# Optimization experiments

Hardware: AMD Instinct MI355X
Metric: run time of the kernel (lower is better)

The kernel has to match this reference:

```python
import jax, jax.numpy as jnp
import numpy as np

N, D, K = 131072, 64, 512
COMMITMENT_COST = 0.25
DECAY = 0.99
EPSILON = 1e-05


def setup_inputs() -> dict:
    key = jax.random.key(0)
    k1, k2, k3 = jax.random.split(key, 3)
    return {
        "inputs": jax.random.normal(k1, (N, D), dtype=jnp.float32),
        "embedding_weight": jax.random.normal(k2, (K, D), dtype=jnp.float32),
        "ema_w": jax.random.normal(k3, (K, D), dtype=jnp.float32),
        "ema_cluster_size": jnp.zeros((K,), dtype=jnp.float32),
    }


def reference(inputs, embedding_weight, ema_w, ema_cluster_size):
    num_embeddings = embedding_weight.shape[0]
    distances = (
        jnp.sum(inputs ** 2, axis=1, keepdims=True)
        + jnp.sum(embedding_weight ** 2, axis=1)
        - 2.0 * jnp.matmul(inputs, embedding_weight.T)
    )
    encoding_indices = jnp.argmin(distances, axis=1)  # [N]
    # dense one-hot (returned by the module); float32 instead of torch double
    encodings = jax.nn.one_hot(encoding_indices, num_embeddings, dtype=jnp.float32)
    # encodings @ W is just a codebook gather
    quantized = jnp.take(embedding_weight, encoding_indices, axis=0)  # [N, D]

    # ---- EMA codebook update (training path; all detached from autodiff) ----
    counts = jax.ops.segment_sum(
        jnp.ones((inputs.shape[0],), dtype=jnp.float32),
        encoding_indices, num_segments=num_embeddings)  # == encodings.sum(0)
    new_cluster_size = ema_cluster_size * DECAY + (1.0 - DECAY) * counts
    n = jnp.sum(new_cluster_size)
    new_cluster_size = (new_cluster_size + EPSILON) / (n + num_embeddings * EPSILON) * n
    # dw = encodings^T @ inputs -> scatter-add of inputs per code
    dw = jax.ops.segment_sum(inputs, encoding_indices, num_segments=num_embeddings)
    new_ema_w = ema_w * DECAY + (1.0 - DECAY) * dw
    new_embedding = new_ema_w / new_cluster_size[:, None]
    new_cluster_size = jax.lax.stop_gradient(new_cluster_size)
    new_ema_w = jax.lax.stop_gradient(new_ema_w)
    new_embedding = jax.lax.stop_gradient(new_embedding)

    # commitment loss (quantized detached)
    e_latent_loss = jnp.mean((jax.lax.stop_gradient(quantized) - inputs) ** 2)
    loss = COMMITMENT_COST * e_latent_loss
    # straight-through estimator
    quantized_st = inputs + jax.lax.stop_gradient(quantized - inputs)

    avg_probs = jnp.mean(encodings, axis=0)
    perplexity = jnp.exp(-jnp.sum(avg_probs * jnp.log(avg_probs + 1e-10)))
    return (loss, quantized_st, perplexity, encodings,
            new_embedding, new_cluster_size, new_ema_w)
```

## Files before the change

kernel.cpp:

```cpp
#include <hip/hip_runtime.h>

#define NROWS 131072
#define DDIM  64
#define KCODE 512

#define QUANT_OFF 1LL
#define PERP_OFF  8388609LL
#define ENC_OFF   8388610LL
#define EMB_OFF   75497474LL
#define CS_OFF    75530242LL
#define EMAW_OFF  75530754LL

#define WS_COUNTS 0
#define WS_NEGWN  512
#define WS_SSE    1024
#define WS_DW     1040
#define WS_ZERO_FLOATS 33808
#define WS_OFF    33808
#define WS_POS    34320
#define WS_IDX    34832
#define WS_BUCKET 165904
#define WS_WHI    296976
#define WS_WMID   313360
#define WS_WLO    329744

using short8 = __attribute__((ext_vector_type(8))) short;
using f32x4  = __attribute__((ext_vector_type(4))) float;

#define MFMA(a, b, c) __builtin_amdgcn_mfma_f32_16x16x32_bf16((a), (b), (c), 0, 0, 0)

__device__ inline unsigned short bf16_rne(float x) {
    unsigned u = __float_as_uint(x);
    unsigned r = u + 0x7FFFu + ((u >> 16) & 1u);
    return (unsigned short)(r >> 16);
}
__device__ inline float bf16_to_f(unsigned short h) {
    return __uint_as_float((unsigned)h << 16);
}
__device__ inline void split3(const float* v, short8& h8, short8& m8, short8& l8) {
#pragma unroll
    for (int j = 0; j < 8; ++j) {
        float x = v[j];
        unsigned short h = bf16_rne(x);
        float m_ = x - bf16_to_f(h);
        unsigned short m = bf16_rne(m_);
        float l_ = m_ - bf16_to_f(m);
        unsigned short l = bf16_rne(l_);
        h8[j] = (short)h; m8[j] = (short)m; l8[j] = (short)l;
    }
}

__global__ void wnorm_kernel(const float* __restrict__ W, float* __restrict__ negwn) {
    int k = threadIdx.x;
    const float4* wr = reinterpret_cast<const float4*>(&W[(size_t)k * DDIM]);
    float s = 0.f;
#pragma unroll
    for (int i = 0; i < DDIM / 4; ++i) {
        float4 v = wr[i];
        s += v.x * v.x + v.y * v.y + v.z * v.z + v.w * v.w;
    }
    negwn[k] = -0.5f * s;
}

__global__ void wprep_kernel(const float* __restrict__ W, ushort* __restrict__ whi,
                             ushort* __restrict__ wmid, ushort* __restrict__ wlo) {
    int t = blockIdx.x * 256 + threadIdx.x;
    int lane = t & 63;
    int code = (t >> 6) * 16 + (lane & 15);
    int kbase = (lane >> 4) * 8;
    int obase = t * 16;
#pragma unroll
    for (int kh = 0; kh < 2; ++kh) {
        float xbuf[8];
#pragma unroll
        for (int j = 0; j < 8; ++j) xbuf[j] = W[code * 64 + kh * 32 + kbase + j];
        short8 h8, m8, l8;
        split3(xbuf, h8, m8, l8);
#pragma unroll
        for (int j = 0; j < 8; ++j) {
            whi[obase + kh * 8 + j]  = (ushort)h8[j];
            wmid[obase + kh * 8 + j] = (ushort)m8[j];
            wlo[obase + kh * 8 + j]  = (ushort)l8[j];
        }
    }
}

__global__ __launch_bounds__(256) void vq_main_kernel(
    const float* __restrict__ X, const ushort* __restrict__ WHI,
    const ushort* __restrict__ WMID, const ushort* __restrict__ WLO,
    const float* __restrict__ negwn, const float* __restrict__ W,
    float* __restrict__ counts, float* __restrict__ sse_g,
    int* __restrict__ idx_out, float* __restrict__ outq, float* __restrict__ enc) {

    __shared__ int rowIdx[128];
    const int tid = threadIdx.x;
    const int wave = tid >> 6, lane = tid & 63;
    const int col = lane & 15, kg = lane >> 4;
    const int row0 = blockIdx.x * 128;
    const int rowbase = row0 + wave * 32;

    short8 xh[2][2], xm[2][2], xl[2][2];
#pragma unroll
    for (int t = 0; t < 2; ++t) {
        int row = rowbase + t * 16 + col;
#pragma unroll
        for (int kh = 0; kh < 2; ++kh) {
            const float4* p = reinterpret_cast<const float4*>(&X[row * 64 + kh * 32 + kg * 8]);
            float4 a = p[0], b = p[1];
            float xbuf[8] = {a.x, a.y, a.z, a.w, b.x, b.y, b.z, b.w};
            split3(xbuf, xh[t][kh], xm[t][kh], xl[t][kh]);
        }
    }

    float bestV[2][4]; int bestC[2][4];
#pragma unroll
    for (int t = 0; t < 2; ++t)
#pragma unroll
        for (int i = 0; i < 4; ++i) { bestV[t][i] = -3.4e38f; bestC[t][i] = 0; }

    for (int c = 0; c < 32; ++c) {
        const short8* ph = reinterpret_cast<const short8*>(&WHI[(c * 64 + lane) * 16]);
        const short8* pm = reinterpret_cast<const short8*>(&WMID[(c * 64 + lane) * 16]);
        const short8* pl = reinterpret_cast<const short8*>(&WLO[(c * 64 + lane) * 16]);
        short8 wh0 = ph[0], wh1 = ph[1];
        short8 wm0 = pm[0], wm1 = pm[1];
        short8 wl0 = pl[0], wl1 = pl[1];
        float wn = negwn[c * 16 + col];
#pragma unroll
        for (int t = 0; t < 2; ++t) {
            f32x4 acc = {0.f, 0.f, 0.f, 0.f};
            acc = MFMA(xh[t][0], wl0, acc); acc = MFMA(xh[t][1], wl1, acc);
            acc = MFMA(xl[t][0], wh0, acc); acc = MFMA(xl[t][1], wh1, acc);
            acc = MFMA(xm[t][0], wm0, acc); acc = MFMA(xm[t][1], wm1, acc);
            acc = MFMA(xh[t][0], wm0, acc); acc = MFMA(xh[t][1], wm1, acc);
            acc = MFMA(xm[t][0], wh0, acc); acc = MFMA(xm[t][1], wh1, acc);
            acc = MFMA(xh[t][0], wh0, acc); acc = MFMA(xh[t][1], wh1, acc);
#pragma unroll
            for (int i = 0; i < 4; ++i) {
                float r = acc[i] + wn;
                if (r > bestV[t][i]) { bestV[t][i] = r; bestC[t][i] = c; }
            }
        }
    }

#pragma unroll
    for (int t = 0; t < 2; ++t)
#pragma unroll
        for (int i = 0; i < 4; ++i) {
            float v = bestV[t][i];
            int ix = bestC[t][i] * 16 + col;
#pragma unroll
            for (int m = 1; m <= 8; m <<= 1) {
                float ov = __shfl_xor(v, m);
                int   oi = __shfl_xor(ix, m);
                if (ov > v || (ov == v && oi < ix)) { v = ov; ix = oi; }
            }
            if (col == 0) rowIdx[wave * 32 + t * 16 + kg * 4 + i] = ix;
        }
    __syncthreads();

    float ssel = 0.f;
    for (int u = tid; u < 128 * 16; u += 256) {
        int r = u >> 4, d4 = (u & 15) << 2;
        int ix = rowIdx[r];
        float4 wv = *reinterpret_cast<const float4*>(&W[ix * 64 + d4]);
        float4 xv = *reinterpret_cast<const float4*>(&X[(size_t)(row0 + r) * 64 + d4]);
        float dx = wv.x - xv.x, dy = wv.y - xv.y, dz = wv.z - xv.z, dw4 = wv.w - xv.w;
        ssel += dx * dx + dy * dy + dz * dz + dw4 * dw4;
        size_t ob = (size_t)(row0 + r) * 64 + d4;
        outq[ob + 0] = xv.x + dx;
        outq[ob + 1] = xv.y + dy;
        outq[ob + 2] = xv.z + dz;
        outq[ob + 3] = xv.w + dw4;
    }
#pragma unroll
    for (int m = 32; m >= 1; m >>= 1) ssel += __shfl_xor(ssel, m);
    if (lane == 0) atomicAdd(sse_g, ssel);

    if (tid < 128) {
        int ix = rowIdx[tid];
        idx_out[row0 + tid] = ix;
        atomicAdd(&counts[ix], 1.0f);
        enc[(size_t)(row0 + tid) * KCODE + ix] = 1.0f;
    }
}

__global__ void prefix_kernel(const float* __restrict__ counts,
                              int* __restrict__ off, int* __restrict__ pos) {
    __shared__ int tmp[512];
    int t = threadIdx.x;
    int c = (int)counts[t];
    tmp[t] = c;
    __syncthreads();
    int val = c;
    for (int s = 1; s < 512; s <<= 1) {
        int add = (t >= s) ? tmp[t - s] : 0;
        __syncthreads();
        val += add; tmp[t] = val;
        __syncthreads();
    }
    int excl = val - c;
    off[t] = excl; pos[t] = excl;
}

__global__ void scatter_kernel(const int* __restrict__ idx, int* __restrict__ pos,
                               int* __restrict__ bucket) {
    int i = blockIdx.x * 256 + threadIdx.x;
    int k = idx[i];
    int p = atomicAdd(&pos[k], 1);
    bucket[p] = (k << 17) | i;
}

__global__ __launch_bounds__(256) void dwsum_kernel(
    const float* __restrict__ X, const int* __restrict__ bucket,
    float* __restrict__ dw) {
    const int lane = threadIdx.x & 63;
    const int gwave = (blockIdx.x * 256 + threadIdx.x) >> 6;
    const int r0 = gwave * 16;
    int v = bucket[r0];
    int k = v >> 17, row = v & 0x1FFFF;
    float acc = 0.f;
#pragma unroll
    for (int i = 0; i < 16; ++i) {
        acc += X[(size_t)row * 64 + lane];
        if (i + 1 < 16) {
            int nv = bucket[r0 + i + 1];
            int nk = nv >> 17, nrow = nv & 0x1FFFF;
            if (nk != k) {
                atomicAdd(&dw[k * 64 + lane], acc);
                acc = 0.f; k = nk;
            }
            row = nrow;
        }
    }
    atomicAdd(&dw[k * 64 + lane], acc);
}

__global__ __launch_bounds__(512) void finalize_kernel(
    const float* __restrict__ ema_w, const float* __restrict__ ema_cs,
    const float* __restrict__ counts, const float* __restrict__ dw,
    const float* __restrict__ sse_g, float* __restrict__ out) {

    __shared__ float red[512];
    __shared__ float cs_sh[512];
    int t = threadIdx.x;

    float cnt = counts[t];
    float raw = ema_cs[t] * 0.99f + 0.01f * cnt;
    red[t] = raw;
    __syncthreads();
    for (int s = 256; s > 0; s >>= 1) {
        if (t < s) red[t] += red[t + s];
        __syncthreads();
    }
    float n = red[0];
    __syncthreads();

    float ncs = (raw + 1e-5f) / (n + (float)KCODE * 1e-5f) * n;
    out[CS_OFF + t] = ncs;
    cs_sh[t] = ncs;

    float avg = cnt / (float)NROWS;
    red[t] = avg * logf(avg + 1e-10f);
    __syncthreads();
    for (int s = 256; s > 0; s >>= 1) {
        if (t < s) red[t] += red[t + s];
        __syncthreads();
    }
    if (t == 0) {
        out[PERP_OFF] = expf(-red[0]);
        out[0] = 0.25f * sse_g[0] / ((float)NROWS * (float)DDIM);
    }
    __syncthreads();

    for (int i = t; i < KCODE * DDIM; i += 512) {
        float ne = ema_w[i] * 0.99f + 0.01f * dw[i];
        out[EMAW_OFF + i] = ne;
        out[EMB_OFF + i] = ne / cs_sh[i >> 6];
    }
}

extern "C" void kernel_launch(void* const* d_in, const int* in_sizes, int n_in,
                              void* d_out, int out_size, void* d_ws, size_t ws_size,
                              hipStream_t stream) {
    const float* X      = (const float*)d_in[0];
    const float* W      = (const float*)d_in[1];
    const float* ema_w  = (const float*)d_in[2];
    const float* ema_cs = (const float*)d_in[3];
    float* out = (float*)d_out;
    float* ws  = (float*)d_ws;

    float*  counts = ws + WS_COUNTS;
    float*  negwn  = ws + WS_NEGWN;
    float*  sse    = ws + WS_SSE;
    float*  dw     = ws + WS_DW;
    int*    off    = (int*)(ws + WS_OFF);
    int*    pos    = (int*)(ws + WS_POS);
    int*    idx    = (int*)(ws + WS_IDX);
    int*    bucket = (int*)(ws + WS_BUCKET);
    ushort* whi    = (ushort*)(ws + WS_WHI);
    ushort* wmid   = (ushort*)(ws + WS_WMID);
    ushort* wlo    = (ushort*)(ws + WS_WLO);

    hipMemsetAsync(d_ws, 0, (size_t)WS_ZERO_FLOATS * sizeof(float), stream);
    hipMemsetAsync(out + ENC_OFF, 0, (size_t)NROWS * KCODE * sizeof(float), stream);

    wnorm_kernel<<<1, 512, 0, stream>>>(W, negwn);
    wprep_kernel<<<8, 256, 0, stream>>>(W, whi, wmid, wlo);
    vq_main_kernel<<<NROWS / 128, 256, 0, stream>>>(X, whi, wmid, wlo, negwn, W,
                                                    counts, sse, idx,
                                                    out + QUANT_OFF, out + ENC_OFF);
    prefix_kernel<<<1, 512, 0, stream>>>(counts, off, pos);
    scatter_kernel<<<NROWS / 256, 256, 0, stream>>>(idx, pos, bucket);
    dwsum_kernel<<<NROWS / 16 / 4, 256, 0, stream>>>(X, bucket, dw);
    finalize_kernel<<<1, 512, 0, stream>>>(ema_w, ema_cs, counts, dw, sse, out);
}
```

Measured before the change: 298.8 us.

## Write one-hot encodings densely in main kernel and merge weight prep kernels

Drops the 256 MiB memset of the encodings buffer and has each block of the main kernel write its own 128x512 one-hot tile in full, using 16-byte nontemporal stores. The base offset is only 8-byte aligned, so the head and tail pairs are handled separately. This removes one full write pass over the largest output. The codebook norm and bf16 split kernels are also merged into a single launch. The cost is extra store work and LDS index comparisons inside the main kernel.

```diff
diff --git a/kernel.cpp b/kernel.cpp
--- a/kernel.cpp
+++ b/kernel.cpp
@@ -26,6 +26,7 @@
 
 using short8 = __attribute__((ext_vector_type(8))) short;
 using f32x4  = __attribute__((ext_vector_type(4))) float;
+using f32x2  = __attribute__((ext_vector_type(2))) float;
 
 #define MFMA(a, b, c) __builtin_amdgcn_mfma_f32_16x16x32_bf16((a), (b), (c), 0, 0, 0)
 
@@ -50,20 +51,23 @@
     }
 }
 
-__global__ void wnorm_kernel(const float* __restrict__ W, float* __restrict__ negwn) {
-    int k = threadIdx.x;
-    const float4* wr = reinterpret_cast<const float4*>(&W[(size_t)k * DDIM]);
-    float s = 0.f;
-#pragma unroll
-    for (int i = 0; i < DDIM / 4; ++i) {
-        float4 v = wr[i];
-        s += v.x * v.x + v.y * v.y + v.z * v.z + v.w * v.w;
-    }
-    negwn[k] = -0.5f * s;
-}
-
-__global__ void wprep_kernel(const float* __restrict__ W, ushort* __restrict__ whi,
-                             ushort* __restrict__ wmid, ushort* __restrict__ wlo) {
+__global__ __launch_bounds__(256) void prep_kernel(
+    const float* __restrict__ W, ushort* __restrict__ whi,
+    ushort* __restrict__ wmid, ushort* __restrict__ wlo,
+    float* __restrict__ negwn) {
+    if (blockIdx.x == 8) {
+        for (int k = threadIdx.x; k < KCODE; k += 256) {
+            const float4* wr = reinterpret_cast<const float4*>(&W[(size_t)k * DDIM]);
+            float s = 0.f;
+#pragma unroll
+            for (int i = 0; i < DDIM / 4; ++i) {
+                float4 v = wr[i];
+                s += v.x * v.x + v.y * v.y + v.z * v.z + v.w * v.w;
+            }
+            negwn[k] = -0.5f * s;
+        }
+        return;
+    }
     int t = blockIdx.x * 256 + threadIdx.x;
     int lane = t & 63;
     int code = (t >> 6) * 16 + (lane & 15);
@@ -181,7 +185,35 @@
         int ix = rowIdx[tid];
         idx_out[row0 + tid] = ix;
         atomicAdd(&counts[ix], 1.0f);
-        enc[(size_t)(row0 + tid) * KCODE + ix] = 1.0f;
+    }
+
+    {
+        float* base = enc + ((size_t)row0 << 9);
+        if (tid == 0) {
+            f32x2 h;
+            h.x = (rowIdx[0] == 0) ? 1.0f : 0.0f;
+            h.y = (rowIdx[0] == 1) ? 1.0f : 0.0f;
+            __builtin_nontemporal_store(h, reinterpret_cast<f32x2*>(base));
+        }
+        if (tid == 255) {
+            f32x2 tl;
+            tl.x = (rowIdx[127] == 510) ? 1.0f : 0.0f;
+            tl.y = (rowIdx[127] == 511) ? 1.0f : 0.0f;
+            __builtin_nontemporal_store(tl, reinterpret_cast<f32x2*>(base + 65534));
+        }
+#pragma unroll 4
+        for (int iter = 0; iter < 64; ++iter) {
+            int k = iter * 256 + tid;
+            if (k < 16383) {
+                int f = 2 + (k << 2);
+                f32x4 v;
+                v.x = (rowIdx[(f + 0) >> 9] == ((f + 0) & 511)) ? 1.0f : 0.0f;
+                v.y = (rowIdx[(f + 1) >> 9] == ((f + 1) & 511)) ? 1.0f : 0.0f;
+                v.z = (rowIdx[(f + 2) >> 9] == ((f + 2) & 511)) ? 1.0f : 0.0f;
+                v.w = (rowIdx[(f + 3) >> 9] == ((f + 3) & 511)) ? 1.0f : 0.0f;
+                __builtin_nontemporal_store(v, reinterpret_cast<f32x4*>(base + f));
+            }
+        }
     }
 }
 
@@ -302,11 +334,9 @@
     ushort* wmid   = (ushort*)(ws + WS_WMID);
     ushort* wlo    = (ushort*)(ws + WS_WLO);
 
-    hipMemsetAsync(d_ws, 0, (size_t)WS_ZERO_FLOATS * sizeof(float), stream);
-    hipMemsetAsync(out + ENC_OFF, 0, (size_t)NROWS * KCODE * sizeof(float), stream);
-
-    wnorm_kernel<<<1, 512, 0, stream>>>(W, negwn);
-    wprep_kernel<<<8, 256, 0, stream>>>(W, whi, wmid, wlo);
+    (void)hipMemsetAsync(d_ws, 0, (size_t)WS_ZERO_FLOATS * sizeof(float), stream);
+
+    prep_kernel<<<9, 256, 0, stream>>>(W, whi, wmid, wlo, negwn);
     vq_main_kernel<<<NROWS / 128, 256, 0, stream>>>(X, whi, wmid, wlo, negwn, W,
                                                     counts, sse, idx,
                                                     out + QUANT_OFF, out + ENC_OFF);
```

Result: faster. 251.4 us, median of 2 (-15.8%).
